# Optimization experiments

Hardware: AMD Instinct MI355X
Metric: run time of the kernel (lower is better)

## Reference

```python
import jax, jax.numpy as jnp
import numpy as np

SEQ_LEN = 16384
HID = 2048


def setup_inputs() -> dict:
    key = jax.random.key(0)
    k1, k2, k3 = jax.random.split(key, 3)
    hidden = jax.random.normal(k1, (1, HID), dtype=jnp.float32)
    encoder_outputs = jax.random.normal(k2, (SEQ_LEN, HID), dtype=jnp.float32)
    # nn.Linear default init ~ U(-1/sqrt(H), 1/sqrt(H)); scale for realism
    W = jax.random.normal(k3, (HID, HID), dtype=jnp.float32) / np.sqrt(HID)
    b = jnp.zeros((HID,), dtype=jnp.float32)
    return {"hidden": hidden, "encoder_outputs": encoder_outputs, "W": W, "b": b}


def reference(hidden, encoder_outputs, W, b):
    # energy_i = Linear(encoder_outputs[i]) = enc @ W^T + b   -> [S, H]
    # attn_energies[i] = hidden . energy_i                   -> [S]
    energy = jnp.einsum('sh,dh->sd', encoder_outputs, W) + b      # [S, H]
    attn_energies = jnp.einsum('sd,d->s', energy, hidden[0])      # [S]
    attn = jax.nn.softmax(attn_energies, axis=0)                  # softmax over seq
    return attn[None, None, :]                                    # [1, 1, S]
```

## Files before the change

kernel.cpp:

```cpp
#include <hip/hip_runtime.h>
#include <math.h>

#define HID 2048
#define SEQ 16384

__global__ __launch_bounds__(256) void compute_v_kernel(
    const float* __restrict__ hidden,
    const float* __restrict__ W,
    float* __restrict__ v)
{
    const int h  = blockIdx.x * 256 + threadIdx.x;
    const int d0 = blockIdx.y * 64;
    float partial = 0.0f;
#pragma unroll 8
    for (int i = 0; i < 64; ++i) {
        const int d = d0 + i;
        partial = fmaf(hidden[d], W[(size_t)d * HID + h], partial);
    }
    atomicAdd(&v[h], partial);
}

#define ROWS_PER_WAVE 4

__global__ __launch_bounds__(256) void compute_energies_kernel(
    const float* __restrict__ enc,
    const float* __restrict__ v,
    float* __restrict__ energies)
{
    const int lane = threadIdx.x & 63;
    const int wave = threadIdx.x >> 6;
    const int row0 = blockIdx.x * (4 * ROWS_PER_WAVE) + wave * ROWS_PER_WAVE;

    const float4* __restrict__ v4 = (const float4*)v;

    float4 vr[8];
#pragma unroll
    for (int j = 0; j < 8; ++j)
        vr[j] = v4[j * 64 + lane];

#pragma unroll
    for (int r = 0; r < ROWS_PER_WAVE; ++r) {
        const int s = row0 + r;
        const float4* __restrict__ row = (const float4*)(enc + (size_t)s * HID);

        float acc = 0.0f;
#pragma unroll
        for (int j = 0; j < 8; ++j) {
            const float4 a = row[j * 64 + lane];
            acc = fmaf(a.x, vr[j].x, acc);
            acc = fmaf(a.y, vr[j].y, acc);
            acc = fmaf(a.z, vr[j].z, acc);
            acc = fmaf(a.w, vr[j].w, acc);
        }
#pragma unroll
        for (int off = 32; off > 0; off >>= 1)
            acc += __shfl_down(acc, off, 64);

        if (lane == 0) energies[s] = acc;
    }
}

__global__ __launch_bounds__(1024) void softmax_kernel(
    const float* __restrict__ energies,
    float* __restrict__ out)
{
    __shared__ float red[16];
    __shared__ float bcast;

    const int tid  = threadIdx.x;
    const int lane = tid & 63;
    const int wave = tid >> 6;

    const float4* __restrict__ e4 = (const float4*)energies;
    float4*       __restrict__ o4 = (float4*)out;

    float vals[16];
    float m = -INFINITY;
#pragma unroll
    for (int i = 0; i < 4; ++i) {
        const float4 a = e4[i * 1024 + tid];
        vals[i * 4 + 0] = a.x;
        vals[i * 4 + 1] = a.y;
        vals[i * 4 + 2] = a.z;
        vals[i * 4 + 3] = a.w;
        m = fmaxf(m, fmaxf(fmaxf(a.x, a.y), fmaxf(a.z, a.w)));
    }

#pragma unroll
    for (int off = 32; off > 0; off >>= 1)
        m = fmaxf(m, __shfl_down(m, off, 64));
    if (lane == 0) red[wave] = m;
    __syncthreads();
    if (tid == 0) {
        float mm = red[0];
#pragma unroll
        for (int i = 1; i < 16; ++i) mm = fmaxf(mm, red[i]);
        bcast = mm;
    }
    __syncthreads();
    const float gmax = bcast;
    __syncthreads();

    float lsum = 0.0f;
#pragma unroll
    for (int i = 0; i < 16; ++i) {
        vals[i] = __expf(vals[i] - gmax);
        lsum += vals[i];
    }
#pragma unroll
    for (int off = 32; off > 0; off >>= 1)
        lsum += __shfl_down(lsum, off, 64);
    if (lane == 0) red[wave] = lsum;
    __syncthreads();
    if (tid == 0) {
        float tot = red[0];
#pragma unroll
        for (int i = 1; i < 16; ++i) tot += red[i];
        bcast = 1.0f / tot;
    }
    __syncthreads();
    const float inv = bcast;

#pragma unroll
    for (int i = 0; i < 4; ++i) {
        float4 o;
        o.x = vals[i * 4 + 0] * inv;
        o.y = vals[i * 4 + 1] * inv;
        o.z = vals[i * 4 + 2] * inv;
        o.w = vals[i * 4 + 3] * inv;
        o4[i * 1024 + tid] = o;
    }
}

extern "C" void kernel_launch(void* const* d_in, const int* in_sizes, int n_in,
                              void* d_out, int out_size, void* d_ws, size_t ws_size,
                              hipStream_t stream)
{
    const float* hidden = (const float*)d_in[0];
    const float* enc    = (const float*)d_in[1];
    const float* W      = (const float*)d_in[2];

    float* out      = (float*)d_out;
    float* v        = (float*)d_ws;
    float* energies = v + HID;

    hipMemsetAsync(v, 0, HID * sizeof(float), stream);

    compute_v_kernel<<<dim3(HID / 256, 32), 256, 0, stream>>>(hidden, W, v);
    compute_energies_kernel<<<SEQ / (4 * ROWS_PER_WAVE), 256, 0, stream>>>(enc, v, energies);
    softmax_kernel<<<1, 1024, 0, stream>>>(energies, out);
}
```

Before: 212.6 us.

## Fuse v, energies and softmax into one cooperative persistent kernel with grid syncs

Replaces three kernel launches with a single cooperative kernel that computes v, the row energies, and a two-pass distributed softmax, separated by grid-wide syncs. The softmax now reduces per-block maxima and sums across the whole grid instead of running on a single 1024-thread block. This removes launch gaps and the serial single-block softmax, but adds three grid.sync barriers and extra global round trips for out. Occupancy is also capped by the grid size the cooperative launch allows.

```diff
diff --git a/kernel.cpp b/kernel.cpp
--- a/kernel.cpp
+++ b/kernel.cpp
@@ -1,134 +1,141 @@
 #include <hip/hip_runtime.h>
+#include <hip/hip_cooperative_groups.h>
 #include <math.h>
+
+namespace cg = cooperative_groups;
 
 #define HID 2048
 #define SEQ 16384
+#define VB   1024
+#define RPB  16
+#define RPW  4
 
-__global__ __launch_bounds__(256) void compute_v_kernel(
+__global__ __launch_bounds__(256, 4) void fused_attn_kernel(
     const float* __restrict__ hidden,
+    const float* __restrict__ enc,
     const float* __restrict__ W,
-    float* __restrict__ v)
+    float* __restrict__ out,
+    float* __restrict__ v,
+    float* __restrict__ energies,
+    float* __restrict__ bmax_arr,
+    float* __restrict__ bsum_arr)
 {
-    const int h  = blockIdx.x * 256 + threadIdx.x;
-    const int d0 = blockIdx.y * 64;
-    float partial = 0.0f;
-#pragma unroll 8
-    for (int i = 0; i < 64; ++i) {
-        const int d = d0 + i;
-        partial = fmaf(hidden[d], W[(size_t)d * HID + h], partial);
-    }
-    atomicAdd(&v[h], partial);
-}
-
-#define ROWS_PER_WAVE 4
-
-__global__ __launch_bounds__(256) void compute_energies_kernel(
-    const float* __restrict__ enc,
-    const float* __restrict__ v,
-    float* __restrict__ energies)
-{
-    const int lane = threadIdx.x & 63;
-    const int wave = threadIdx.x >> 6;
-    const int row0 = blockIdx.x * (4 * ROWS_PER_WAVE) + wave * ROWS_PER_WAVE;
-
-    const float4* __restrict__ v4 = (const float4*)v;
-
-    float4 vr[8];
-#pragma unroll
-    for (int j = 0; j < 8; ++j)
-        vr[j] = v4[j * 64 + lane];
-
-#pragma unroll
-    for (int r = 0; r < ROWS_PER_WAVE; ++r) {
-        const int s = row0 + r;
-        const float4* __restrict__ row = (const float4*)(enc + (size_t)s * HID);
-
-        float acc = 0.0f;
-#pragma unroll
-        for (int j = 0; j < 8; ++j) {
-            const float4 a = row[j * 64 + lane];
-            acc = fmaf(a.x, vr[j].x, acc);
-            acc = fmaf(a.y, vr[j].y, acc);
-            acc = fmaf(a.z, vr[j].z, acc);
-            acc = fmaf(a.w, vr[j].w, acc);
-        }
-#pragma unroll
-        for (int off = 32; off > 0; off >>= 1)
-            acc += __shfl_down(acc, off, 64);
-
-        if (lane == 0) energies[s] = acc;
-    }
-}
-
-__global__ __launch_bounds__(1024) void softmax_kernel(
-    const float* __restrict__ energies,
-    float* __restrict__ out)
-{
-    __shared__ float red[16];
-    __shared__ float bcast;
+    cg::grid_group grid = cg::this_grid();
 
     const int tid  = threadIdx.x;
     const int lane = tid & 63;
     const int wave = tid >> 6;
+    const int nb   = gridDim.x;
 
-    const float4* __restrict__ e4 = (const float4*)energies;
-    float4*       __restrict__ o4 = (float4*)out;
+    for (int vb = blockIdx.x; vb < VB; vb += nb) {
+        const int h  = (vb & 7) * 256 + tid;
+        const int d0 = (vb >> 3) * 16;
+        float partial = 0.0f;
+#pragma unroll
+        for (int i = 0; i < 16; ++i) {
+            const int d = d0 + i;
+            partial = fmaf(hidden[d], W[(size_t)d * HID + h], partial);
+        }
+        atomicAdd(&v[h], partial);
+    }
+    grid.sync();
 
-    float vals[16];
-    float m = -INFINITY;
+    __shared__ float se[RPB];
+    __shared__ float sred[4];
+    __shared__ float sb;
+
+    {
+        const float4* __restrict__ v4 = (const float4*)v;
+        float4 vr[8];
 #pragma unroll
-    for (int i = 0; i < 4; ++i) {
-        const float4 a = e4[i * 1024 + tid];
-        vals[i * 4 + 0] = a.x;
-        vals[i * 4 + 1] = a.y;
-        vals[i * 4 + 2] = a.z;
-        vals[i * 4 + 3] = a.w;
-        m = fmaxf(m, fmaxf(fmaxf(a.x, a.y), fmaxf(a.z, a.w)));
+        for (int j = 0; j < 8; ++j)
+            vr[j] = v4[j * 64 + lane];
+
+        for (int vb = blockIdx.x; vb < VB; vb += nb) {
+            const int row0 = vb * RPB + wave * RPW;
+#pragma unroll
+            for (int r = 0; r < RPW; ++r) {
+                const int s = row0 + r;
+                const float4* __restrict__ row = (const float4*)(enc + (size_t)s * HID);
+                float acc = 0.0f;
+#pragma unroll
+                for (int j = 0; j < 8; ++j) {
+                    const float4 a = row[j * 64 + lane];
+                    acc = fmaf(a.x, vr[j].x, acc);
+                    acc = fmaf(a.y, vr[j].y, acc);
+                    acc = fmaf(a.z, vr[j].z, acc);
+                    acc = fmaf(a.w, vr[j].w, acc);
+                }
+#pragma unroll
+                for (int off = 32; off > 0; off >>= 1)
+                    acc += __shfl_down(acc, off, 64);
+                if (lane == 0) {
+                    energies[s] = acc;
+                    se[wave * RPW + r] = acc;
+                }
+            }
+            __syncthreads();
+            if (tid == 0) {
+                float m = se[0];
+#pragma unroll
+                for (int i = 1; i < RPB; ++i) m = fmaxf(m, se[i]);
+                bmax_arr[vb] = m;
+            }
+            __syncthreads();
+        }
     }
+    grid.sync();
 
+    {
+        const float4 bm = ((const float4*)bmax_arr)[tid];
+        float m = fmaxf(fmaxf(bm.x, bm.y), fmaxf(bm.z, bm.w));
 #pragma unroll
-    for (int off = 32; off > 0; off >>= 1)
-        m = fmaxf(m, __shfl_down(m, off, 64));
-    if (lane == 0) red[wave] = m;
-    __syncthreads();
-    if (tid == 0) {
-        float mm = red[0];
+        for (int off = 32; off > 0; off >>= 1)
+            m = fmaxf(m, __shfl_down(m, off, 64));
+        if (lane == 0) sred[wave] = m;
+        __syncthreads();
+        if (tid == 0)
+            sb = fmaxf(fmaxf(sred[0], sred[1]), fmaxf(sred[2], sred[3]));
+        __syncthreads();
+        const float gmax = sb;
+
+        for (int vb = blockIdx.x; vb < VB; vb += nb) {
+            float ex = 0.0f;
+            if (tid < RPB) {
+                const int s = vb * RPB + tid;
+                ex = __expf(energies[s] - gmax);
+                out[s] = ex;
+            }
+            if (wave == 0) {
+                float sum = ex;
 #pragma unroll
-        for (int i = 1; i < 16; ++i) mm = fmaxf(mm, red[i]);
-        bcast = mm;
+                for (int off = 32; off > 0; off >>= 1)
+                    sum += __shfl_down(sum, off, 64);
+                if (lane == 0) bsum_arr[vb] = sum;
+            }
+        }
     }
-    __syncthreads();
-    const float gmax = bcast;
-    __syncthreads();
+    grid.sync();
 
-    float lsum = 0.0f;
+    {
+        const float4 bs = ((const float4*)bsum_arr)[tid];
+        float ssum = bs.x + bs.y + bs.z + bs.w;
 #pragma unroll
-    for (int i = 0; i < 16; ++i) {
-        vals[i] = __expf(vals[i] - gmax);
-        lsum += vals[i];
-    }
-#pragma unroll
-    for (int off = 32; off > 0; off >>= 1)
-        lsum += __shfl_down(lsum, off, 64);
-    if (lane == 0) red[wave] = lsum;
-    __syncthreads();
-    if (tid == 0) {
-        float tot = red[0];
-#pragma unroll
-        for (int i = 1; i < 16; ++i) tot += red[i];
-        bcast = 1.0f / tot;
-    }
-    __syncthreads();
-    const float inv = bcast;
+        for (int off = 32; off > 0; off >>= 1)
+            ssum += __shfl_down(ssum, off, 64);
+        if (lane == 0) sred[wave] = ssum;
+        __syncthreads();
+        if (tid == 0)
+            sb = 1.0f / (sred[0] + sred[1] + sred[2] + sred[3]);
+        __syncthreads();
+        const float inv = sb;
 
-#pragma unroll
-    for (int i = 0; i < 4; ++i) {
-        float4 o;
-        o.x = vals[i * 4 + 0] * inv;
-        o.y = vals[i * 4 + 1] * inv;
-        o.z = vals[i * 4 + 2] * inv;
-        o.w = vals[i * 4 + 3] * inv;
-        o4[i * 1024 + tid] = o;
+        for (int vb = blockIdx.x; vb < VB; vb += nb) {
+            if (tid < RPB) {
+                const int s = vb * RPB + tid;
+                out[s] *= inv;
+            }
+        }
     }
 }
 
@@ -143,10 +150,26 @@
     float* out      = (float*)d_out;
     float* v        = (float*)d_ws;
     float* energies = v + HID;
+    float* bmax_arr = energies + SEQ;
+    float* bsum_arr = bmax_arr + VB;
 
     hipMemsetAsync(v, 0, HID * sizeof(float), stream);
 
-    compute_v_kernel<<<dim3(HID / 256, 32), 256, 0, stream>>>(hidden, W, v);
-    compute_energies_kernel<<<SEQ / (4 * ROWS_PER_WAVE), 256, 0, stream>>>(enc, v, energies);
-    softmax_kernel<<<1, 1024, 0, stream>>>(energies, out);
+    static int grid_blocks = 0;
+    if (grid_blocks == 0) {
+        int per_cu = 0;
+        hipOccupancyMaxActiveBlocksPerMultiprocessor(&per_cu, fused_attn_kernel, 256, 0);
+        int dev = 0;
+        hipGetDevice(&dev);
+        hipDeviceProp_t prop;
+        hipGetDeviceProperties(&prop, dev);
+        int total = per_cu * prop.multiProcessorCount;
+        if (total < 1) total = 256;
+        grid_blocks = total < VB ? total : VB;
+    }
+
+    void* args[] = {(void*)&hidden, (void*)&enc, (void*)&W, (void*)&out,
+                    (void*)&v, (void*)&energies, (void*)&bmax_arr, (void*)&bsum_arr};
+    hipLaunchCooperativeKernel((void*)fused_attn_kernel, dim3(grid_blocks), dim3(256),
+                               args, 0, stream);
 }
```

After: 389.9 us. +83.4%, slower.

## Parallelize softmax across blocks with atomic max/sum and vectorize v computation

Applied to the files above, without the earlier changes.

Replaces the single-block softmax with a multi-block scheme. The global max is computed inside the energies kernel using an order-preserving unsigned encoding and atomicMax, then separate exp+sum and normalize kernels run across 16 blocks. The v computation now loads float4 rows of W with a 2x128 grid and four atomics per thread. This adds a kernel launch and extra global atomics in exchange for removing the serial one-block softmax tail.

```diff
diff --git a/kernel.cpp b/kernel.cpp
--- a/kernel.cpp
+++ b/kernel.cpp
@@ -4,20 +4,41 @@
 #define HID 2048
 #define SEQ 16384
 
+__device__ __forceinline__ unsigned enc_f32(float f) {
+    unsigned u = __float_as_uint(f);
+    return (u & 0x80000000u) ? ~u : (u | 0x80000000u);
+}
+__device__ __forceinline__ float dec_f32(unsigned e) {
+    unsigned u = (e & 0x80000000u) ? (e ^ 0x80000000u) : ~e;
+    return __uint_as_float(u);
+}
+
 __global__ __launch_bounds__(256) void compute_v_kernel(
     const float* __restrict__ hidden,
     const float* __restrict__ W,
     float* __restrict__ v)
 {
-    const int h  = blockIdx.x * 256 + threadIdx.x;
-    const int d0 = blockIdx.y * 64;
-    float partial = 0.0f;
-#pragma unroll 8
-    for (int i = 0; i < 64; ++i) {
+    const int h4 = blockIdx.x * 256 + threadIdx.x;
+    const int d0 = blockIdx.y * 16;
+
+    const float4* __restrict__ W4 = (const float4*)W;
+
+    float4 p = make_float4(0.f, 0.f, 0.f, 0.f);
+#pragma unroll
+    for (int i = 0; i < 16; ++i) {
         const int d = d0 + i;
-        partial = fmaf(hidden[d], W[(size_t)d * HID + h], partial);
+        const float  hd = hidden[d];
+        const float4 w  = W4[(size_t)d * (HID / 4) + h4];
+        p.x = fmaf(hd, w.x, p.x);
+        p.y = fmaf(hd, w.y, p.y);
+        p.z = fmaf(hd, w.z, p.z);
+        p.w = fmaf(hd, w.w, p.w);
     }
-    atomicAdd(&v[h], partial);
+    float* dst = v + 4 * h4;
+    atomicAdd(dst + 0, p.x);
+    atomicAdd(dst + 1, p.y);
+    atomicAdd(dst + 2, p.z);
+    atomicAdd(dst + 3, p.w);
 }
 
 #define ROWS_PER_WAVE 4
@@ -25,8 +46,11 @@
 __global__ __launch_bounds__(256) void compute_energies_kernel(
     const float* __restrict__ enc,
     const float* __restrict__ v,
-    float* __restrict__ energies)
+    float* __restrict__ energies,
+    unsigned* __restrict__ gmax_u)
 {
+    __shared__ float sred[4];
+
     const int lane = threadIdx.x & 63;
     const int wave = threadIdx.x >> 6;
     const int row0 = blockIdx.x * (4 * ROWS_PER_WAVE) + wave * ROWS_PER_WAVE;
@@ -38,6 +62,7 @@
     for (int j = 0; j < 8; ++j)
         vr[j] = v4[j * 64 + lane];
 
+    float wmax = -INFINITY;
 #pragma unroll
     for (int r = 0; r < ROWS_PER_WAVE; ++r) {
         const int s = row0 + r;
@@ -56,80 +81,62 @@
         for (int off = 32; off > 0; off >>= 1)
             acc += __shfl_down(acc, off, 64);
 
-        if (lane == 0) energies[s] = acc;
+        if (lane == 0) {
+            energies[s] = acc;
+            wmax = fmaxf(wmax, acc);
+        }
+    }
+
+    if (lane == 0) sred[wave] = wmax;
+    __syncthreads();
+    if (threadIdx.x == 0) {
+        const float bmax = fmaxf(fmaxf(sred[0], sred[1]), fmaxf(sred[2], sred[3]));
+        atomicMax(gmax_u, enc_f32(bmax));
     }
 }
 
-__global__ __launch_bounds__(1024) void softmax_kernel(
+__global__ __launch_bounds__(256) void exp_sum_kernel(
     const float* __restrict__ energies,
+    const unsigned* __restrict__ gmax_u,
+    float* __restrict__ gsum,
     float* __restrict__ out)
 {
-    __shared__ float red[16];
-    __shared__ float bcast;
+    __shared__ float sred[4];
 
     const int tid  = threadIdx.x;
     const int lane = tid & 63;
     const int wave = tid >> 6;
+    const int idx  = blockIdx.x * 256 + tid;
 
-    const float4* __restrict__ e4 = (const float4*)energies;
-    float4*       __restrict__ o4 = (float4*)out;
+    const float gmax = dec_f32(*gmax_u);
 
-    float vals[16];
-    float m = -INFINITY;
-#pragma unroll
-    for (int i = 0; i < 4; ++i) {
-        const float4 a = e4[i * 1024 + tid];
-        vals[i * 4 + 0] = a.x;
-        vals[i * 4 + 1] = a.y;
-        vals[i * 4 + 2] = a.z;
-        vals[i * 4 + 3] = a.w;
-        m = fmaxf(m, fmaxf(fmaxf(a.x, a.y), fmaxf(a.z, a.w)));
-    }
+    const float4 a = ((const float4*)energies)[idx];
+    float4 ex;
+    ex.x = __expf(a.x - gmax);
+    ex.y = __expf(a.y - gmax);
+    ex.z = __expf(a.z - gmax);
+    ex.w = __expf(a.w - gmax);
+    ((float4*)out)[idx] = ex;
 
+    float sum = ex.x + ex.y + ex.z + ex.w;
 #pragma unroll
     for (int off = 32; off > 0; off >>= 1)
-        m = fmaxf(m, __shfl_down(m, off, 64));
-    if (lane == 0) red[wave] = m;
+        sum += __shfl_down(sum, off, 64);
+    if (lane == 0) sred[wave] = sum;
     __syncthreads();
-    if (tid == 0) {
-        float mm = red[0];
-#pragma unroll
-        for (int i = 1; i < 16; ++i) mm = fmaxf(mm, red[i]);
-        bcast = mm;
-    }
-    __syncthreads();
-    const float gmax = bcast;
-    __syncthreads();
+    if (tid == 0)
+        atomicAdd(gsum, sred[0] + sred[1] + sred[2] + sred[3]);
+}
 
-    float lsum = 0.0f;
-#pragma unroll
-    for (int i = 0; i < 16; ++i) {
-        vals[i] = __expf(vals[i] - gmax);
-        lsum += vals[i];
-    }
-#pragma unroll
-    for (int off = 32; off > 0; off >>= 1)
-        lsum += __shfl_down(lsum, off, 64);
-    if (lane == 0) red[wave] = lsum;
-    __syncthreads();
-    if (tid == 0) {
-        float tot = red[0];
-#pragma unroll
-        for (int i = 1; i < 16; ++i) tot += red[i];
-        bcast = 1.0f / tot;
-    }
-    __syncthreads();
-    const float inv = bcast;
-
-#pragma unroll
-    for (int i = 0; i < 4; ++i) {
-        float4 o;
-        o.x = vals[i * 4 + 0] * inv;
-        o.y = vals[i * 4 + 1] * inv;
-        o.z = vals[i * 4 + 2] * inv;
-        o.w = vals[i * 4 + 3] * inv;
-        o4[i * 1024 + tid] = o;
-    }
+__global__ __launch_bounds__(256) void normalize_kernel(
+    const float* __restrict__ gsum,
+    float* __restrict__ out)
+{
+    const int idx = blockIdx.x * 256 + threadIdx.x;
+    const float inv = 1.0f / *gsum;
+    float4 o = ((float4*)out)[idx];
+    o.x *= inv; o.y *= inv; o.z *= inv; o.w *= inv;
+    ((float4*)out)[idx] = o;
 }
 
 extern "C" void kernel_launch(void* const* d_in, const int* in_sizes, int n_in,
@@ -141,12 +148,15 @@
     const float* W      = (const float*)d_in[2];
 
     float* out      = (float*)d_out;
-    float* v        = (float*)d_ws;
-    float* energies = v + HID;
+    float*    v      = (float*)d_ws;
+    unsigned* gmax_u = (unsigned*)(v + HID);
+    float*    gsum   = (float*)(gmax_u + 1);
+    float*    energies = v + HID + 4;
 
-    hipMemsetAsync(v, 0, HID * sizeof(float), stream);
+    hipMemsetAsync(v, 0, (HID + 4) * sizeof(float), stream);
 
-    compute_v_kernel<<<dim3(HID / 256, 32), 256, 0, stream>>>(hidden, W, v);
-    compute_energies_kernel<<<SEQ / (4 * ROWS_PER_WAVE), 256, 0, stream>>>(enc, v, energies);
-    softmax_kernel<<<1, 1024, 0, stream>>>(energies, out);
+    compute_v_kernel<<<dim3(2, 128), 256, 0, stream>>>(hidden, W, v);
+    compute_energies_kernel<<<SEQ / (4 * ROWS_PER_WAVE), 256, 0, stream>>>(enc, v, energies, gmax_u);
+    exp_sum_kernel<<<SEQ / 1024, 256, 0, stream>>>(energies, gmax_u, gsum, out);
+    normalize_kernel<<<SEQ / 1024, 256, 0, stream>>>(gsum, out);
 }
```

After: 222.9 us. 4.9% more time.
